# Kernel tuning notes

Hardware: AMD Instinct MI355X
Metric: run time of the kernel (lower is better)

The kernel has to match this reference:

```python
import jax, jax.numpy as jnp
import numpy as np

COMMITMENT_COST = 0.25


def setup_inputs() -> dict:
    key = jax.random.key(0)
    k1, k2 = jax.random.split(key)
    x = jax.random.normal(k1, (32, 1024, 512), dtype=jnp.float32)
    codebook = jax.random.normal(k2, (8192, 512), dtype=jnp.float32)
    return {"x": x, "codebook": codebook}


def reference(x, codebook):
    D = codebook.shape[1]
    flat = x.reshape(-1, D)                                   # [N, D]
    # squared L2 distances: ||f||^2 + ||c||^2 - 2 f c^T
    distances = (
        jnp.sum(flat * flat, axis=1, keepdims=True)
        + jnp.sum(codebook * codebook, axis=1)
        - 2.0 * jnp.matmul(flat, codebook.T)                   # [N, K]
    )
    encoding_indices = jnp.argmin(distances, axis=1)           # [N]
    quantized = codebook[encoding_indices].reshape(x.shape)    # [.., D]
    commitment_loss = COMMITMENT_COST * jnp.mean(
        (jax.lax.stop_gradient(quantized) - x) ** 2
    )
    # straight-through estimator
    quantized_st = x + jax.lax.stop_gradient(quantized - x)
    return (quantized_st, commitment_loss)
```

## Files before the change

### kernel.cpp

```cpp
#include <hip/hip_runtime.h>
#include <stdint.h>

#define N_TOT 32768
#define DDIM  512
#define KCB   8192
#define NSPLIT 4
#define COLS_SPLIT (KCB / NSPLIT)
#define BN 256
#define BC 256
#define BKD 64
#define NTILES (COLS_SPLIT / BC)
#define NSTEPS (NTILES * 8)
#define MARGIN 0.15f

#define RB3 32
#define RP3 32
#define RSLOTS (RGRID3 / RP3)
#define RGRID3 2048

typedef _Float16 half8 __attribute__((ext_vector_type(8)));
typedef float    floatx4 __attribute__((ext_vector_type(4)));

typedef const __attribute__((address_space(1))) unsigned int* gas_ptr;
typedef __attribute__((address_space(3))) unsigned int* las_ptr;
__device__ __forceinline__ void gld_lds16(void* l, const void* g) {
    __builtin_amdgcn_global_load_lds((gas_ptr)g, (las_ptr)l, 16, 0, 0);
}

__device__ __forceinline__ unsigned long long shfl_xor_u64(unsigned long long v, int m) {
    unsigned int lo = (unsigned int)v, hi = (unsigned int)(v >> 32);
    lo = __shfl_xor(lo, m, 64);
    hi = __shfl_xor(hi, m, 64);
    return ((unsigned long long)hi << 32) | lo;
}

__global__ __launch_bounds__(256) void convert_x_kernel(
    const float* __restrict__ x, _Float16* __restrict__ xh) {
    size_t i = ((size_t)blockIdx.x * 256 + threadIdx.x) * 8;
    float4 v0 = *(const float4*)(x + i);
    float4 v1 = *(const float4*)(x + i + 4);
    half8 h;
    h[0] = (_Float16)v0.x; h[1] = (_Float16)v0.y; h[2] = (_Float16)v0.z; h[3] = (_Float16)v0.w;
    h[4] = (_Float16)v1.x; h[5] = (_Float16)v1.y; h[6] = (_Float16)v1.z; h[7] = (_Float16)v1.w;
    *(half8*)(xh + i) = h;
}

__global__ __launch_bounds__(256) void convert_cb_kernel(
    const float* __restrict__ cb, _Float16* __restrict__ cbh, float* __restrict__ cnorm) {
    int row = blockIdx.x * 4 + (threadIdx.x >> 6);
    int lane = threadIdx.x & 63;
    const float* src = cb + (size_t)row * DDIM + lane * 8;
    float4 v0 = *(const float4*)src;
    float4 v1 = *(const float4*)(src + 4);
    half8 h;
    h[0] = (_Float16)v0.x; h[1] = (_Float16)v0.y; h[2] = (_Float16)v0.z; h[3] = (_Float16)v0.w;
    h[4] = (_Float16)v1.x; h[5] = (_Float16)v1.y; h[6] = (_Float16)v1.z; h[7] = (_Float16)v1.w;
    *(half8*)(cbh + (size_t)row * DDIM + lane * 8) = h;
    float s = v0.x*v0.x + v0.y*v0.y + v0.z*v0.z + v0.w*v0.w
            + v1.x*v1.x + v1.y*v1.y + v1.z*v1.z + v1.w*v1.w;
#pragma unroll
    for (int off = 32; off > 0; off >>= 1) s += __shfl_down(s, off, 64);
    if (lane == 0) cnorm[row] = s;
}

__global__ __launch_bounds__(512, 2) void gemm_argmin_kernel(
    const _Float16* __restrict__ xh, const _Float16* __restrict__ cbh,
    const float* __restrict__ cnorm,
    float* __restrict__ sb1, int* __restrict__ si1, float* __restrict__ sb2) {

    __shared__ __align__(16) _Float16 smem[65536];
    char* smemb = (char*)smem;

    const int tid = threadIdx.x;
    const int wave = tid >> 6;
    const int lane = tid & 63;
    const int rowPart = wave >> 1;
    const int colPart = wave & 1;
    const int l15 = lane & 15;
    const int quad = lane >> 4;

    const int orig = blockIdx.x;
    const int wg = (orig & 7) * 64 + (orig >> 3);
    const int bx = wg & 127;
    const int by = wg >> 7;
    const int row0 = bx * BN;
    const int colBase = by * COLS_SPLIT;

    int voff[4];
#pragma unroll
    for (int r = 0; r < 4; ++r) {
        int c = wave * 256 + r * 64 + lane;
        int ar = c >> 3;
        int q  = (c & 7) ^ (ar & 7);
        voff[r] = (ar << 9) + q * 8;
    }
    const _Float16* aptr = xh + ((size_t)row0 << 9);
    const _Float16* bptr = cbh + ((size_t)colBase << 9);

    int aaddr[4], baddr[8];
#pragma unroll
    for (int i = 0; i < 4; ++i) {
        int rr = rowPart * 64 + i * 16 + l15;
        int qa = quad ^ (rr & 7);
        aaddr[i] = rr * 128 + qa * 16;
    }
#pragma unroll
    for (int j = 0; j < 8; ++j) {
        int cc = colPart * 128 + j * 16 + l15;
        int qb = quad ^ (cc & 7);
        baddr[j] = 32768 + cc * 128 + qb * 16;
    }

    float b1[16], b2[16];
    int   i1[16];
#pragma unroll
    for (int s = 0; s < 16; ++s) { b1[s] = 3.402823466e38f; b2[s] = 3.402823466e38f; i1[s] = 0; }

#define STAGE(parv, boffu, d0v) do {                                            \
        _Float16* Asb = smem + (parv) * 32768;                                  \
        _Float16* Bsb = Asb + 16384;                                            \
        _Pragma("unroll")                                                       \
        for (int r = 0; r < 4; ++r) {                                           \
            gld_lds16(Asb + (wave * 256 + r * 64) * 8,                          \
                      aptr + (d0v) + voff[r]);                                  \
            gld_lds16(Bsb + (wave * 256 + r * 64) * 8,                          \
                      bptr + (boffu) + (d0v) + voff[r]);                        \
        }                                                                       \
    } while (0)

    floatx4 acc[4][8];
#pragma unroll
    for (int i = 0; i < 4; ++i)
#pragma unroll
        for (int j = 0; j < 8; ++j)
            acc[i][j] = (floatx4){0.f, 0.f, 0.f, 0.f};

    STAGE(0, 0, 0);
    __syncthreads();

    int pofs = 0;
    for (int s = 0; s < NSTEPS; ++s) {
        if (s + 1 < NSTEPS) {
            STAGE((s + 1) & 1, ((s + 1) >> 3) << 17, ((s + 1) & 7) * BKD);
        }
#pragma unroll
        for (int kh = 0; kh < 2; ++kh) {
            half8 af[4], bf[8];
#pragma unroll
            for (int i = 0; i < 4; ++i)
                af[i] = *(const half8*)(smemb + (pofs + (aaddr[i] ^ (kh << 6))));
#pragma unroll
            for (int j = 0; j < 8; ++j)
                bf[j] = *(const half8*)(smemb + (pofs + (baddr[j] ^ (kh << 6))));
#pragma unroll
            for (int i = 0; i < 4; ++i)
#pragma unroll
                for (int j = 0; j < 8; ++j)
                    acc[i][j] = __builtin_amdgcn_mfma_f32_16x16x32_f16(
                        af[i], bf[j], acc[i][j], 0, 0, 0);
        }
        if ((s & 7) == 7) {
            const int col0 = colBase + (s >> 3) * BC;
#pragma unroll
            for (int j = 0; j < 8; ++j) {
                int col = col0 + colPart * 128 + j * 16 + l15;
                float cn = cnorm[col];
#pragma unroll
                for (int i = 0; i < 4; ++i) {
#pragma unroll
                    for (int r = 0; r < 4; ++r) {
                        float sc = fmaf(-2.0f, acc[i][j][r], cn);
                        int slot = i * 4 + r;
                        if (sc < b1[slot]) { b2[slot] = b1[slot]; b1[slot] = sc; i1[slot] = col; }
                        else if (sc < b2[slot]) b2[slot] = sc;
                    }
                }
            }
#pragma unroll
            for (int i = 0; i < 4; ++i)
#pragma unroll
                for (int j = 0; j < 8; ++j)
                    acc[i][j] = (floatx4){0.f, 0.f, 0.f, 0.f};
        }
        pofs ^= 65536;
        __syncthreads();
    }
#undef STAGE

#pragma unroll
    for (int m = 1; m < 16; m <<= 1) {
#pragma unroll
        for (int s = 0; s < 16; ++s) {
            float ob1 = __shfl_xor(b1[s], m, 64);
            float ob2 = __shfl_xor(b2[s], m, 64);
            int   oi1 = __shfl_xor(i1[s], m, 64);
            if (ob1 < b1[s] || (ob1 == b1[s] && oi1 < i1[s])) {
                b2[s] = fminf(b1[s], ob2);
                b1[s] = ob1; i1[s] = oi1;
            } else {
                b2[s] = fminf(b2[s], ob1);
            }
        }
    }

    float* mb1 = (float*)smem;
    float* mb2 = mb1 + 512;
    int*   mi1 = (int*)(mb2 + 512);
    if (l15 == 0) {
#pragma unroll
        for (int s = 0; s < 16; ++s) {
            int row = rowPart * 64 + (s >> 2) * 16 + quad * 4 + (s & 3);
            mb1[colPart * 256 + row] = b1[s];
            mb2[colPart * 256 + row] = b2[s];
            mi1[colPart * 256 + row] = i1[s];
        }
    }
    __syncthreads();
    if (tid < 256) {
        float a1 = mb1[tid], a2 = mb2[tid]; int ai = mi1[tid];
        float c1 = mb1[256 + tid], c2 = mb2[256 + tid]; int ci = mi1[256 + tid];
        float r1, r2; int ri;
        if (c1 < a1 || (c1 == a1 && ci < ai)) { r1 = c1; ri = ci; r2 = fminf(a1, c2); }
        else { r1 = a1; ri = ai; r2 = fminf(a2, c1); }
        size_t o = (size_t)by * N_TOT + row0 + tid;
        sb1[o] = r1; si1[o] = ri; sb2[o] = r2;
    }
}

__global__ __launch_bounds__(256) void merge_kernel(
    const float* __restrict__ sb1, const int* __restrict__ si1, const float* __restrict__ sb2,
    int* __restrict__ indices, int* __restrict__ flags,
    int* __restrict__ list, int* __restrict__ count,
    unsigned long long* __restrict__ result) {
    int n = blockIdx.x * 256 + threadIdx.x;
    float b1 = sb1[n]; int i1 = si1[n]; float b2 = sb2[n];
#pragma unroll
    for (int s = 1; s < NSPLIT; ++s) {
        float ob1 = sb1[(size_t)s * N_TOT + n];
        int   oi1 = si1[(size_t)s * N_TOT + n];
        float ob2 = sb2[(size_t)s * N_TOT + n];
        if (ob1 < b1 || (ob1 == b1 && oi1 < i1)) { b2 = fminf(b1, ob2); b1 = ob1; i1 = oi1; }
        else b2 = fminf(b2, ob1);
    }
    indices[n] = i1;
    result[n] = 0xFFFFFFFFFFFFFFFFull;
    int f = (b2 - b1 < MARGIN) ? 1 : 0;
    flags[n] = f;
    if (f) { int pos = atomicAdd(count, 1); list[pos] = n; }
}

__global__ __launch_bounds__(256) void repair3_kernel(
    const float* __restrict__ x, const float* __restrict__ cb,
    const float* __restrict__ cnorm, const int* __restrict__ list,
    const int* __restrict__ count, unsigned long long* __restrict__ result) {
    __shared__ __align__(16) float xs[RB3][512];
    __shared__ unsigned long long red[RB3][4];
    const int tid = threadIdx.x;
    const int lane = tid & 63;
    const int wv = tid >> 6;
    const int part = blockIdx.x & (RP3 - 1);
    const int slot0 = blockIdx.x >> 5;
    const int cnt = *count;
    const int nbatch = (cnt + RB3 - 1) / RB3;
    const int k = part * 256 + tid;
    const float cn = cnorm[k];
    const float* crow = cb + (size_t)k * 512;

    for (int batch = slot0; batch < nbatch; batch += RSLOTS) {
        const int rb = min(RB3, cnt - batch * RB3);
        __syncthreads();
        for (int t = tid; t < rb * 128; t += 256) {
            int b = t >> 7, d4 = t & 127;
            int n = list[batch * RB3 + b];
            ((float4*)xs[b])[d4] = ((const float4*)(x + ((size_t)n << 9)))[d4];
        }
        __syncthreads();

        float d0[RB3], d1[RB3], d2[RB3], d3[RB3];
#pragma unroll
        for (int b = 0; b < RB3; ++b) { d0[b] = 0.f; d1[b] = 0.f; d2[b] = 0.f; d3[b] = 0.f; }

        for (int t = 0; t < 512; t += 16) {
            float4 c0 = *(const float4*)(crow + t);
            float4 c1 = *(const float4*)(crow + t + 4);
            float4 c2 = *(const float4*)(crow + t + 8);
            float4 c3 = *(const float4*)(crow + t + 12);
#pragma unroll
            for (int b = 0; b < RB3; ++b) {
                float4 x0 = *(const float4*)&xs[b][t];
                float4 x1 = *(const float4*)&xs[b][t + 4];
                float4 x2 = *(const float4*)&xs[b][t + 8];
                float4 x3 = *(const float4*)&xs[b][t + 12];
                d0[b] = fmaf(c0.x, x0.x, d0[b]);  d0[b] = fmaf(c0.y, x0.y, d0[b]);
                d0[b] = fmaf(c0.z, x0.z, d0[b]);  d0[b] = fmaf(c0.w, x0.w, d0[b]);
                d1[b] = fmaf(c1.x, x1.x, d1[b]);  d1[b] = fmaf(c1.y, x1.y, d1[b]);
                d1[b] = fmaf(c1.z, x1.z, d1[b]);  d1[b] = fmaf(c1.w, x1.w, d1[b]);
                d2[b] = fmaf(c2.x, x2.x, d2[b]);  d2[b] = fmaf(c2.y, x2.y, d2[b]);
                d2[b] = fmaf(c2.z, x2.z, d2[b]);  d2[b] = fmaf(c2.w, x2.w, d2[b]);
                d3[b] = fmaf(c3.x, x3.x, d3[b]);  d3[b] = fmaf(c3.y, x3.y, d3[b]);
                d3[b] = fmaf(c3.z, x3.z, d3[b]);  d3[b] = fmaf(c3.w, x3.w, d3[b]);
            }
        }

#pragma unroll
        for (int b = 0; b < RB3; ++b) {
            float s = cn - 2.f * ((d0[b] + d1[b]) + (d2[b] + d3[b]));
            unsigned int sb = __float_as_uint(s);
            sb = (sb & 0x80000000u) ? ~sb : (sb | 0x80000000u);
            unsigned long long p = ((unsigned long long)sb << 32) | (unsigned int)k;
#pragma unroll
            for (int m = 32; m > 0; m >>= 1) {
                unsigned long long o = shfl_xor_u64(p, m);
                if (o < p) p = o;
            }
            if (lane == 0) red[b][wv] = p;
        }
        __syncthreads();
        if (tid < RB3) {
            unsigned long long p = red[tid][0];
            if (red[tid][1] < p) p = red[tid][1];
            if (red[tid][2] < p) p = red[tid][2];
            if (red[tid][3] < p) p = red[tid][3];
            if (tid < rb) {
                int n = list[batch * RB3 + tid];
                atomicMin(&result[n], p);
            }
        }
    }
}

__global__ __launch_bounds__(256) void fixup_kernel(
    const int* __restrict__ flags, const unsigned long long* __restrict__ result,
    int* __restrict__ indices) {
    int n = blockIdx.x * 256 + threadIdx.x;
    if (flags[n]) indices[n] = (int)(result[n] & 0xFFFFFFFFu);
}

__global__ void cnorm_kernel(const float* __restrict__ cb, float* __restrict__ cnorm) {
    int wave = (blockIdx.x * blockDim.x + threadIdx.x) >> 6;
    int lane = threadIdx.x & 63;
    if (wave >= KCB) return;
    const float* row = cb + (size_t)wave * DDIM;
    float s = 0.f;
#pragma unroll
    for (int j = 0; j < DDIM / 64; ++j) { float v = row[lane + 64 * j]; s += v * v; }
#pragma unroll
    for (int off = 32; off > 0; off >>= 1) s += __shfl_down(s, off, 64);
    if (lane == 0) cnorm[wave] = s;
}

#define FBN 64
#define FBD 32
#define FLDA (FBN + 4)
__global__ __launch_bounds__(256) void argmin_fp32_kernel(
    const float* __restrict__ x, const float* __restrict__ cb,
    const float* __restrict__ cnorm, int* __restrict__ indices) {
    __shared__ float As[FBD][FLDA];
    __shared__ float Bs[FBD][FLDA];
    __shared__ float redv[FBN][16];
    __shared__ int   redi[FBN][16];
    const int tid = threadIdx.x;
    const int tx = tid & 15, ty = tid >> 4;
    const int row0 = blockIdx.x * FBN;
    float best[4]; int bidx[4];
#pragma unroll
    for (int i = 0; i < 4; ++i) { best[i] = 3.402823466e+38f; bidx[i] = KCB; }
    for (int k0 = 0; k0 < KCB; k0 += 64) {
        float acc[4][4] = {};
        for (int d0 = 0; d0 < DDIM; d0 += FBD) {
#pragma unroll
            for (int t = 0; t < 2; ++t) {
                int q = tid + t * 256, rr = q >> 3, dq = q & 7;
                float4 v = *(const float4*)(x + (size_t)(row0 + rr) * DDIM + d0 + dq * 4);
                As[dq*4+0][rr] = v.x; As[dq*4+1][rr] = v.y; As[dq*4+2][rr] = v.z; As[dq*4+3][rr] = v.w;
                float4 w = *(const float4*)(cb + (size_t)(k0 + rr) * DDIM + d0 + dq * 4);
                Bs[dq*4+0][rr] = w.x; Bs[dq*4+1][rr] = w.y; Bs[dq*4+2][rr] = w.z; Bs[dq*4+3][rr] = w.w;
            }
            __syncthreads();
#pragma unroll
            for (int d = 0; d < FBD; ++d) {
                float4 av = *(const float4*)&As[d][ty * 4];
                float4 bv = *(const float4*)&Bs[d][tx * 4];
                float a[4] = {av.x, av.y, av.z, av.w}, b[4] = {bv.x, bv.y, bv.z, bv.w};
#pragma unroll
                for (int i = 0; i < 4; ++i)
#pragma unroll
                    for (int j = 0; j < 4; ++j) acc[i][j] += a[i] * b[j];
            }
            __syncthreads();
        }
#pragma unroll
        for (int j = 0; j < 4; ++j) {
            int k = k0 + tx * 4 + j;
            float cn = cnorm[k];
#pragma unroll
            for (int i = 0; i < 4; ++i) {
                float s = cn - 2.0f * acc[i][j];
                if (s < best[i] || (s == best[i] && k < bidx[i])) { best[i] = s; bidx[i] = k; }
            }
        }
    }
#pragma unroll
    for (int i = 0; i < 4; ++i) { redv[ty*4+i][tx] = best[i]; redi[ty*4+i][tx] = bidx[i]; }
    __syncthreads();
    if (tid < FBN) {
        float bv = redv[tid][0]; int bi = redi[tid][0];
#pragma unroll
        for (int t = 1; t < 16; ++t) {
            float v = redv[tid][t]; int ii = redi[tid][t];
            if (v < bv || (v == bv && ii < bi)) { bv = v; bi = ii; }
        }
        indices[row0 + tid] = bi;
    }
}

__global__ __launch_bounds__(256) void output_kernel(
    const float* __restrict__ x, const float* __restrict__ cb,
    const int* __restrict__ indices, float* __restrict__ out,
    float* __restrict__ loss_acc) {
    size_t base = ((size_t)blockIdx.x * blockDim.x + threadIdx.x) * 16;
    int n = (int)(base >> 9);
    int d = (int)(base & 511);
    int idx = indices[n];
    const float* cr = cb + (size_t)idx * DDIM + d;
    const float* xr = x + base;
    float* orow = out + base;
    float lsum = 0.f;
#pragma unroll
    for (int t = 0; t < 4; ++t) {
        float4 q  = *(const float4*)(cr + t * 4);
        float4 xv = *(const float4*)(xr + t * 4);
        float dx0 = q.x - xv.x, dx1 = q.y - xv.y, dx2 = q.z - xv.z, dx3 = q.w - xv.w;
        float4 o;
        o.x = xv.x + dx0; o.y = xv.y + dx1; o.z = xv.z + dx2; o.w = xv.w + dx3;
        *(float4*)(orow + t * 4) = o;
        lsum += dx0*dx0 + dx1*dx1 + dx2*dx2 + dx3*dx3;
    }
#pragma unroll
    for (int off = 32; off > 0; off >>= 1) lsum += __shfl_down(lsum, off, 64);
    __shared__ float wsum[4];
    int lane = threadIdx.x & 63, wv = threadIdx.x >> 6;
    if (lane == 0) wsum[wv] = lsum;
    __syncthreads();
    if (threadIdx.x == 0) atomicAdd(loss_acc, wsum[0] + wsum[1] + wsum[2] + wsum[3]);
}

__global__ void finalize_kernel(const float* __restrict__ loss_acc, float* __restrict__ out_loss) {
    *out_loss = (*loss_acc) * (0.25f / (float)((size_t)N_TOT * DDIM));
}

extern "C" void kernel_launch(void* const* d_in, const int* in_sizes, int n_in,
                              void* d_out, int out_size, void* d_ws, size_t ws_size,
                              hipStream_t stream) {
    const float* x  = (const float*)d_in[0];
    const float* cb = (const float*)d_in[1];
    float* out = (float*)d_out;

    char* ws = (char*)d_ws;
    float* loss_acc = (float*)ws;
    int*   count    = (int*)(ws + 8);
    int*   indices  = (int*)(ws + 256);
    int*   flags    = (int*)(ws + 256 + 131072);
    float* cnorm    = (float*)(ws + 256 + 2 * 131072);
    int*   list     = (int*)(ws + 256 + 2 * 131072 + 32768);
    unsigned long long* result =
        (unsigned long long*)(ws + 256 + 3 * 131072 + 32768);
    size_t off = 256 + 3 * 131072 + 32768 + 262144;
    _Float16* xh  = (_Float16*)(ws + off);
    _Float16* cbh = (_Float16*)(ws + off + (size_t)N_TOT * DDIM * 2);
    size_t soff = off + (size_t)N_TOT * DDIM * 2 + (size_t)KCB * DDIM * 2;
    float* sb1 = (float*)(ws + soff);
    int*   si1 = (int*)(ws + soff + (size_t)NSPLIT * N_TOT * 4);
    float* sb2 = (float*)(ws + soff + (size_t)NSPLIT * N_TOT * 8);
    size_t need = soff + (size_t)NSPLIT * N_TOT * 12;

    hipMemsetAsync(ws, 0, 16, stream);
    if (ws_size >= need) {
        convert_x_kernel<<<(N_TOT * DDIM) / (256 * 8), 256, 0, stream>>>(x, xh);
        convert_cb_kernel<<<KCB / 4, 256, 0, stream>>>(cb, cbh, cnorm);
        gemm_argmin_kernel<<<(N_TOT / BN) * NSPLIT, 512, 0, stream>>>(
            xh, cbh, cnorm, sb1, si1, sb2);
        merge_kernel<<<N_TOT / 256, 256, 0, stream>>>(sb1, si1, sb2, indices, flags,
                                                      list, count, result);
        repair3_kernel<<<RGRID3, 256, 0, stream>>>(x, cb, cnorm, list, count, result);
        fixup_kernel<<<N_TOT / 256, 256, 0, stream>>>(flags, result, indices);
    } else {
        cnorm_kernel<<<KCB / 4, 256, 0, stream>>>(cb, cnorm);
        argmin_fp32_kernel<<<N_TOT / FBN, 256, 0, stream>>>(x, cb, cnorm, indices);
    }
    output_kernel<<<((size_t)N_TOT * DDIM) / (256 * 16), 256, 0, stream>>>(
        x, cb, indices, out, loss_acc);
    finalize_kernel<<<1, 1, 0, stream>>>(loss_acc, out + (size_t)N_TOT * DDIM);
}
```

Baseline: 821.3 us.

## Prefetch two stages ahead with explicit vmcnt waits and raw barriers

Restructures the double-buffered GEMM main loop so two stages are issued before the loop. Each iteration waits only on the older stage's global-to-LDS loads using a partial vmcnt count, then issues the load for stage s+2 after a barrier. The full __syncthreads is replaced with raw s_barrier plus sched_barrier fences, and s_setprio is raised around the MFMA block. The intent is deeper overlap of memory loads with compute and less synchronization overhead. It relies on the exact count of outstanding loads (8 per stage), which is fragile if the load count changes.

```diff
diff --git a/kernel.cpp b/kernel.cpp
--- a/kernel.cpp
+++ b/kernel.cpp
@@ -116,15 +116,17 @@
 #pragma unroll
     for (int s = 0; s < 16; ++s) { b1[s] = 3.402823466e38f; b2[s] = 3.402823466e38f; i1[s] = 0; }
 
-#define STAGE(parv, boffu, d0v) do {                                            \
-        _Float16* Asb = smem + (parv) * 32768;                                  \
+#define STAGE(st) do {                                                          \
+        _Float16* Asb = smem + ((st) & 1) * 32768;                              \
         _Float16* Bsb = Asb + 16384;                                            \
+        const int boffu = ((st) >> 3) << 17;          \
+        const int d0v   = ((st) & 7) * BKD;                                     \
         _Pragma("unroll")                                                       \
         for (int r = 0; r < 4; ++r) {                                           \
             gld_lds16(Asb + (wave * 256 + r * 64) * 8,                          \
-                      aptr + (d0v) + voff[r]);                                  \
+                      aptr + d0v + voff[r]);                                    \
             gld_lds16(Bsb + (wave * 256 + r * 64) * 8,                          \
-                      bptr + (boffu) + (d0v) + voff[r]);                        \
+                      bptr + boffu + d0v + voff[r]);                            \
         }                                                                       \
     } while (0)
 
@@ -135,23 +137,30 @@
         for (int j = 0; j < 8; ++j)
             acc[i][j] = (floatx4){0.f, 0.f, 0.f, 0.f};
 
-    STAGE(0, 0, 0);
-    __syncthreads();
-
-    int pofs = 0;
+    STAGE(0);
+    STAGE(1);
+
     for (int s = 0; s < NSTEPS; ++s) {
         if (s + 1 < NSTEPS) {
-            STAGE((s + 1) & 1, ((s + 1) >> 3) << 17, ((s + 1) & 7) * BKD);
-        }
+            asm volatile("s_waitcnt vmcnt(8)" ::: "memory");
+        } else {
+            asm volatile("s_waitcnt vmcnt(0)" ::: "memory");
+        }
+        __builtin_amdgcn_sched_barrier(0);
+        __builtin_amdgcn_s_barrier();
+        __builtin_amdgcn_sched_barrier(0);
+
+        const char* Ab = smemb + (s & 1) * 65536;
+        __builtin_amdgcn_s_setprio(1);
 #pragma unroll
         for (int kh = 0; kh < 2; ++kh) {
             half8 af[4], bf[8];
 #pragma unroll
             for (int i = 0; i < 4; ++i)
-                af[i] = *(const half8*)(smemb + (pofs + (aaddr[i] ^ (kh << 6))));
+                af[i] = *(const half8*)(Ab + (aaddr[i] ^ (kh << 6)));
 #pragma unroll
             for (int j = 0; j < 8; ++j)
-                bf[j] = *(const half8*)(smemb + (pofs + (baddr[j] ^ (kh << 6))));
+                bf[j] = *(const half8*)(Ab + (baddr[j] ^ (kh << 6)));
 #pragma unroll
             for (int i = 0; i < 4; ++i)
 #pragma unroll
@@ -159,6 +168,8 @@
                     acc[i][j] = __builtin_amdgcn_mfma_f32_16x16x32_f16(
                         af[i], bf[j], acc[i][j], 0, 0, 0);
         }
+        __builtin_amdgcn_s_setprio(0);
+
         if ((s & 7) == 7) {
             const int col0 = colBase + (s >> 3) * BC;
 #pragma unroll
@@ -182,10 +193,16 @@
                 for (int j = 0; j < 8; ++j)
                     acc[i][j] = (floatx4){0.f, 0.f, 0.f, 0.f};
         }
-        pofs ^= 65536;
-        __syncthreads();
+
+        __builtin_amdgcn_s_barrier();
+        __builtin_amdgcn_sched_barrier(0);
+        if (s + 2 < NSTEPS) {
+            STAGE(s + 2);
+        }
     }
 #undef STAGE
+
+    __syncthreads();
 
 #pragma unroll
     for (int m = 1; m < 16; m <<= 1) {
```

New measurement: 836.2 us. No clear change (+1.8%).
